# Optimization experiments

Hardware: AMD Instinct MI355X
Metric: run time of the kernel (lower is better)

## Reference

```python
import jax, jax.numpy as jnp
import numpy as np

EPS = 1e-12  # tf.math.l2_normalize epsilon

def _l2_normalize(v, axis):
    sq = jnp.sum(v * v, axis=axis, keepdims=True)
    return v * jax.lax.rsqrt(jnp.maximum(sq, EPS))

def setup_inputs() -> dict:
    key = jax.random.key(0)
    k1, k2, k3 = jax.random.split(key, 3)
    B, H, Wd, Cin, K = 16, 64, 64, 512, 64  # K == dim (required by the source's broadcast)
    x = jax.random.normal(k1, (B, H, Wd, Cin), dtype=jnp.float32)
    W = jax.random.normal(k2, (Cin, K), dtype=jnp.float32) * (1.0 / np.sqrt(Cin))
    b = jnp.zeros((K,), dtype=jnp.float32)
    C = jax.random.uniform(k3, (1, 1, 1, K, K), dtype=jnp.float32)  # [1,1,1,dim,clusters]
    return {"x": x, "W": W, "b": b, "C": C}

def reference(x, W, b, C):
    # 1x1 conv: per-pixel linear projection to cluster logits. NOTE: the
    # original code overwrites x with the conv output, so the VLAD residual
    # is built from these logits, not the input features (faithful to source).
    f = jnp.einsum('bhwc,ck->bhwk', x, W) + b            # [B,H,W,K]
    s = jax.nn.softmax(f, axis=-1)                        # soft assignment over clusters
    # a: [B,H,W,1,K], residual: [B,H,W,dim,K] with dim==K
    v = s[..., None, :] * (f[..., :, None] + C)           # [B,H,W,dim,K]
    v = jnp.sum(v, axis=(1, 2))                           # [B,dim,K]
    v = jnp.transpose(v, (0, 2, 1))                       # [B,K,dim]
    # postnorm=True: intra-normalize per cluster, then global L2 of flattened
    v = _l2_normalize(v, axis=-1)
    flat = v.reshape(v.shape[0], -1)                      # [B, K*dim]
    return _l2_normalize(flat, axis=-1)
```

## Files before the change

kernel.cpp:

```cpp
#include <hip/hip_runtime.h>

#define NB 16
#define HW 4096
#define CIN 512
#define KCL 64
#define BP 128
#define NCHUNK (HW / BP)
#define WT_STRIDE 520
#define FS_STRIDE 68

#define SMEM_FLOATS 17664

typedef short s16x8 __attribute__((ext_vector_type(8)));
typedef float f32x4 __attribute__((ext_vector_type(4)));

__device__ __forceinline__ unsigned short f2bf(float f) {
    unsigned u = __builtin_bit_cast(unsigned, f);
    u += 0x7fffu + ((u >> 16) & 1u);
    return (unsigned short)(u >> 16);
}

__global__ void vlad_prep(const float* __restrict__ Wm, float* __restrict__ A_g,
                          unsigned short* __restrict__ Wt_g)
{
    const int i = blockIdx.x * 256 + threadIdx.x;
    if (i < NB * KCL * KCL + NB * KCL) A_g[i] = 0.f;
    if (i < CIN * KCL) {
        const int k = i >> 6;
        const int n = i & 63;
        Wt_g[n * 512 + k] = f2bf(Wm[i]);
    }
}

__global__ __launch_bounds__(256, 2) void vlad_main(
    const float* __restrict__ x, const unsigned short* __restrict__ Wt_g,
    const float* __restrict__ bv, float* __restrict__ A_g,
    float* __restrict__ sumS_g)
{
    __shared__ float smem_f[SMEM_FLOATS];
    unsigned short* wt = (unsigned short*)smem_f;
    float* fs = smem_f;
    float* ss = smem_f + BP * FS_STRIDE;
    float* sums4 = smem_f + 2 * BP * FS_STRIDE;

    const int t = threadIdx.x;
    const int b = blockIdx.x >> 5;
    const int chunk = blockIdx.x & 31;
    const int pb = b * HW + chunk * BP;

    {
        const int n = t >> 2;
        const int kc = (t & 3) * 128;
        const unsigned short* src = Wt_g + n * 512 + kc;
        unsigned short* dst = wt + n * WT_STRIDE + kc;
#pragma unroll
        for (int i = 0; i < 16; ++i)
            *(float4*)(dst + i * 8) = *(const float4*)(src + i * 8);
    }
    __syncthreads();

    const int wid = t >> 6;
    const int lane = t & 63;
    const int col = lane & 15;
    const int g = lane >> 4;
    const int wpix = pb + wid * 32;

    f32x4 acc[2][4];
#pragma unroll
    for (int mt = 0; mt < 2; ++mt)
#pragma unroll
        for (int nt = 0; nt < 4; ++nt) acc[mt][nt] = (f32x4){0.f, 0.f, 0.f, 0.f};

    const float* xr = x + (size_t)(wpix + col) * CIN + g * 8;
    const unsigned short* wb = wt + col * WT_STRIDE + g * 8;

#pragma unroll
    for (int kk = 0; kk < 16; ++kk) {
        const int k0 = kk * 32;
        s16x8 a[2];
#pragma unroll
        for (int mt = 0; mt < 2; ++mt) {
            const float4 u0 = *(const float4*)(xr + mt * (16 * CIN) + k0);
            const float4 u1 = *(const float4*)(xr + mt * (16 * CIN) + k0 + 4);
            a[mt][0] = (short)f2bf(u0.x); a[mt][1] = (short)f2bf(u0.y);
            a[mt][2] = (short)f2bf(u0.z); a[mt][3] = (short)f2bf(u0.w);
            a[mt][4] = (short)f2bf(u1.x); a[mt][5] = (short)f2bf(u1.y);
            a[mt][6] = (short)f2bf(u1.z); a[mt][7] = (short)f2bf(u1.w);
        }
#pragma unroll
        for (int nt = 0; nt < 4; ++nt) {
            const s16x8 bfr = *(const s16x8*)(wb + nt * (16 * WT_STRIDE) + k0);
            acc[0][nt] = __builtin_amdgcn_mfma_f32_16x16x32_bf16(a[0], bfr, acc[0][nt], 0, 0, 0);
            acc[1][nt] = __builtin_amdgcn_mfma_f32_16x16x32_bf16(a[1], bfr, acc[1][nt], 0, 0, 0);
        }
    }
    __syncthreads();

    float bj[4];
#pragma unroll
    for (int nt = 0; nt < 4; ++nt) bj[nt] = bv[nt * 16 + col];

#pragma unroll
    for (int mt = 0; mt < 2; ++mt)
#pragma unroll
        for (int r = 0; r < 4; ++r) {
            float v0 = acc[mt][0][r] + bj[0];
            float v1 = acc[mt][1][r] + bj[1];
            float v2 = acc[mt][2][r] + bj[2];
            float v3 = acc[mt][3][r] + bj[3];
            float m = fmaxf(fmaxf(v0, v1), fmaxf(v2, v3));
            m = fmaxf(m, __shfl_xor(m, 1));
            m = fmaxf(m, __shfl_xor(m, 2));
            m = fmaxf(m, __shfl_xor(m, 4));
            m = fmaxf(m, __shfl_xor(m, 8));
            const float e0 = __expf(v0 - m);
            const float e1 = __expf(v1 - m);
            const float e2 = __expf(v2 - m);
            const float e3 = __expf(v3 - m);
            float lsum = e0 + e1 + e2 + e3;
            lsum += __shfl_xor(lsum, 1);
            lsum += __shfl_xor(lsum, 2);
            lsum += __shfl_xor(lsum, 4);
            lsum += __shfl_xor(lsum, 8);
            const float rl = 1.0f / lsum;
            const int p = wid * 32 + mt * 16 + g * 4 + r;
            float* fr = fs + p * FS_STRIDE + col;
            fr[0] = v0; fr[16] = v1; fr[32] = v2; fr[48] = v3;
            float* sr = ss + p * FS_STRIDE + col;
            sr[0] = e0 * rl; sr[16] = e1 * rl; sr[32] = e2 * rl; sr[48] = e3 * rl;
        }
    __syncthreads();

    {
        const int c64 = t & 63;
        const int pr = (t >> 6) * 32;
        float sp = 0.f;
#pragma unroll 8
        for (int p = 0; p < 32; ++p) sp += ss[(pr + p) * FS_STRIDE + c64];
        sums4[(t >> 6) * 64 + c64] = sp;
    }

    const int td = t & 15;
    const int tk = t >> 4;
    float Aacc[4][4];
#pragma unroll
    for (int di = 0; di < 4; ++di)
#pragma unroll
        for (int kj = 0; kj < 4; ++kj) Aacc[di][kj] = 0.f;

#pragma unroll 4
    for (int p = 0; p < BP; ++p) {
        const float4 fd = *(const float4*)(fs + p * FS_STRIDE + td * 4);
        const float4 sk = *(const float4*)(ss + p * FS_STRIDE + tk * 4);
        const float fdv[4] = {fd.x, fd.y, fd.z, fd.w};
        const float skv[4] = {sk.x, sk.y, sk.z, sk.w};
#pragma unroll
        for (int di = 0; di < 4; ++di)
#pragma unroll
            for (int kj = 0; kj < 4; ++kj)
                Aacc[di][kj] = fmaf(fdv[di], skv[kj], Aacc[di][kj]);
    }
    __syncthreads();

    float* Ab = A_g + b * (KCL * KCL);
#pragma unroll
    for (int di = 0; di < 4; ++di)
#pragma unroll
        for (int kj = 0; kj < 4; ++kj)
            atomicAdd(Ab + (td * 4 + di) * KCL + tk * 4 + kj, Aacc[di][kj]);

    if (t < 64) {
        const float s4 = sums4[t] + sums4[64 + t] + sums4[128 + t] + sums4[192 + t];
        atomicAdd(sumS_g + b * KCL + t, s4);
    }
}

__global__ __launch_bounds__(256) void vlad_finalize(
    const float* __restrict__ A_g, const float* __restrict__ sumS_g,
    const float* __restrict__ Cm, float* __restrict__ out)
{
    __shared__ float red[4];
    const int b = blockIdx.x;
    const int t = threadIdx.x;
    const int k = t >> 2;
    const int dg = t & 3;
    const float sS = sumS_g[b * 64 + k];
    float v[16];
    float ssq = 0.f;
#pragma unroll
    for (int i = 0; i < 16; ++i) {
        const int d = dg * 16 + i;
        const float val = A_g[((size_t)b * 64 + d) * 64 + k] + Cm[d * 64 + k] * sS;
        v[i] = val;
        ssq += val * val;
    }
    ssq += __shfl_xor(ssq, 1);
    ssq += __shfl_xor(ssq, 2);
    const float rn = rsqrtf(fmaxf(ssq, 1e-12f));
    float gpart = 0.f;
#pragma unroll
    for (int i = 0; i < 16; ++i) {
        v[i] *= rn;
        gpart += v[i] * v[i];
    }
#pragma unroll
    for (int m = 1; m < 64; m <<= 1) gpart += __shfl_xor(gpart, m);
    if ((t & 63) == 0) red[t >> 6] = gpart;
    __syncthreads();
    const float gsq = red[0] + red[1] + red[2] + red[3];
    const float gr = rsqrtf(fmaxf(gsq, 1e-12f));
    float* o = out + (size_t)b * 4096 + k * 64 + dg * 16;
#pragma unroll
    for (int i = 0; i < 16; ++i) o[i] = v[i] * gr;
}

extern "C" void kernel_launch(void* const* d_in, const int* in_sizes, int n_in,
                              void* d_out, int out_size, void* d_ws, size_t ws_size,
                              hipStream_t stream)
{
    const float* x  = (const float*)d_in[0];
    const float* Wm = (const float*)d_in[1];
    const float* bv = (const float*)d_in[2];
    const float* Cm = (const float*)d_in[3];

    float* A_g = (float*)d_ws;
    float* sumS_g = A_g + NB * KCL * KCL;
    unsigned short* Wt_g = (unsigned short*)(sumS_g + NB * KCL);

    const int nz = NB * KCL * KCL + NB * KCL;
    vlad_prep<<<(nz + 255) / 256, 256, 0, stream>>>(Wm, A_g, Wt_g);
    vlad_main<<<NB * NCHUNK, 256, 0, stream>>>(x, Wt_g, bv, A_g, sumS_g);
    vlad_finalize<<<NB, 256, 0, stream>>>(A_g, sumS_g, Cm, (float*)d_out);
}
```

Measured before the change: 228.3 us.

## Use MFMA for per-chunk VLAD aggregation with bf16 transposed LDS tiles

```diff
diff --git a/kernel.cpp b/kernel.cpp
--- a/kernel.cpp
+++ b/kernel.cpp
@@ -1,17 +1,16 @@
 #include <hip/hip_runtime.h>
+#include <hip/hip_bf16.h>
 
 #define NB 16
 #define HW 4096
 #define CIN 512
 #define KCL 64
 #define BP 128
-#define NCHUNK (HW / BP)
-#define WT_STRIDE 520
-#define FS_STRIDE 68
-
-#define SMEM_FLOATS 17664
+#define NCHUNK 32
+#define PSTRIDE 136
 
 typedef short s16x8 __attribute__((ext_vector_type(8)));
+typedef int   i32x4 __attribute__((ext_vector_type(4)));
 typedef float f32x4 __attribute__((ext_vector_type(4)));
 
 __device__ __forceinline__ unsigned short f2bf(float f) {
@@ -20,44 +19,37 @@
     return (unsigned short)(u >> 16);
 }
 
+__device__ __forceinline__ unsigned pk2(float lo, float hi) {
+    __hip_bfloat162 h = __float22bfloat162_rn(make_float2(lo, hi));
+    unsigned r;
+    __builtin_memcpy(&r, &h, 4);
+    return r;
+}
+
 __global__ void vlad_prep(const float* __restrict__ Wm, float* __restrict__ A_g,
                           unsigned short* __restrict__ Wt_g)
 {
     const int i = blockIdx.x * 256 + threadIdx.x;
     if (i < NB * KCL * KCL + NB * KCL) A_g[i] = 0.f;
     if (i < CIN * KCL) {
-        const int k = i >> 6;
+        const int c = i >> 6;
         const int n = i & 63;
-        Wt_g[n * 512 + k] = f2bf(Wm[i]);
-    }
-}
-
-__global__ __launch_bounds__(256, 2) void vlad_main(
+        Wt_g[n * 512 + c] = f2bf(Wm[i]);
+    }
+}
+
+__global__ __launch_bounds__(256, 4) void vlad_main(
     const float* __restrict__ x, const unsigned short* __restrict__ Wt_g,
     const float* __restrict__ bv, float* __restrict__ A_g,
     float* __restrict__ sumS_g)
 {
-    __shared__ float smem_f[SMEM_FLOATS];
-    unsigned short* wt = (unsigned short*)smem_f;
-    float* fs = smem_f;
-    float* ss = smem_f + BP * FS_STRIDE;
-    float* sums4 = smem_f + 2 * BP * FS_STRIDE;
+    __shared__ unsigned short ft[KCL * PSTRIDE];
+    __shared__ unsigned short st[KCL * PSTRIDE];
 
     const int t = threadIdx.x;
     const int b = blockIdx.x >> 5;
     const int chunk = blockIdx.x & 31;
     const int pb = b * HW + chunk * BP;
-
-    {
-        const int n = t >> 2;
-        const int kc = (t & 3) * 128;
-        const unsigned short* src = Wt_g + n * 512 + kc;
-        unsigned short* dst = wt + n * WT_STRIDE + kc;
-#pragma unroll
-        for (int i = 0; i < 16; ++i)
-            *(float4*)(dst + i * 8) = *(const float4*)(src + i * 8);
-    }
-    __syncthreads();
 
     const int wid = t >> 6;
     const int lane = t & 63;
@@ -71,34 +63,38 @@
 #pragma unroll
         for (int nt = 0; nt < 4; ++nt) acc[mt][nt] = (f32x4){0.f, 0.f, 0.f, 0.f};
 
-    const float* xr = x + (size_t)(wpix + col) * CIN + g * 8;
-    const unsigned short* wb = wt + col * WT_STRIDE + g * 8;
+    const float* xr0 = x + (size_t)(wpix + col) * CIN + g * 8;
+    const float* xr1 = xr0 + 16 * CIN;
+    const unsigned short* wbase = Wt_g + col * 512 + g * 8;
 
 #pragma unroll
     for (int kk = 0; kk < 16; ++kk) {
         const int k0 = kk * 32;
-        s16x8 a[2];
-#pragma unroll
-        for (int mt = 0; mt < 2; ++mt) {
-            const float4 u0 = *(const float4*)(xr + mt * (16 * CIN) + k0);
-            const float4 u1 = *(const float4*)(xr + mt * (16 * CIN) + k0 + 4);
-            a[mt][0] = (short)f2bf(u0.x); a[mt][1] = (short)f2bf(u0.y);
-            a[mt][2] = (short)f2bf(u0.z); a[mt][3] = (short)f2bf(u0.w);
-            a[mt][4] = (short)f2bf(u1.x); a[mt][5] = (short)f2bf(u1.y);
-            a[mt][6] = (short)f2bf(u1.z); a[mt][7] = (short)f2bf(u1.w);
+        const float4 u00 = *(const float4*)(xr0 + k0);
+        const float4 u01 = *(const float4*)(xr0 + k0 + 4);
+        const float4 u10 = *(const float4*)(xr1 + k0);
+        const float4 u11 = *(const float4*)(xr1 + k0 + 4);
+        s16x8 wf[4];
+#pragma unroll
+        for (int nt = 0; nt < 4; ++nt)
+            wf[nt] = *(const s16x8*)(wbase + nt * (16 * 512) + k0);
+        const i32x4 a0i = {(int)pk2(u00.x, u00.y), (int)pk2(u00.z, u00.w),
+                           (int)pk2(u01.x, u01.y), (int)pk2(u01.z, u01.w)};
+        const i32x4 a1i = {(int)pk2(u10.x, u10.y), (int)pk2(u10.z, u10.w),
+                           (int)pk2(u11.x, u11.y), (int)pk2(u11.z, u11.w)};
+        const s16x8 a0 = __builtin_bit_cast(s16x8, a0i);
+        const s16x8 a1 = __builtin_bit_cast(s16x8, a1i);
+#pragma unroll
+        for (int nt = 0; nt < 4; ++nt) {
+            acc[0][nt] = __builtin_amdgcn_mfma_f32_16x16x32_bf16(a0, wf[nt], acc[0][nt], 0, 0, 0);
+            acc[1][nt] = __builtin_amdgcn_mfma_f32_16x16x32_bf16(a1, wf[nt], acc[1][nt], 0, 0, 0);
         }
-#pragma unroll
-        for (int nt = 0; nt < 4; ++nt) {
-            const s16x8 bfr = *(const s16x8*)(wb + nt * (16 * WT_STRIDE) + k0);
-            acc[0][nt] = __builtin_amdgcn_mfma_f32_16x16x32_bf16(a[0], bfr, acc[0][nt], 0, 0, 0);
-            acc[1][nt] = __builtin_amdgcn_mfma_f32_16x16x32_bf16(a[1], bfr, acc[1][nt], 0, 0, 0);
-        }
-    }
-    __syncthreads();
+    }
 
     float bj[4];
 #pragma unroll
     for (int nt = 0; nt < 4; ++nt) bj[nt] = bv[nt * 16 + col];
+    float ssum[4] = {0.f, 0.f, 0.f, 0.f};
 
 #pragma unroll
     for (int mt = 0; mt < 2; ++mt)
@@ -123,56 +119,52 @@
             lsum += __shfl_xor(lsum, 4);
             lsum += __shfl_xor(lsum, 8);
             const float rl = 1.0f / lsum;
+            const float s0 = e0 * rl, s1 = e1 * rl, s2 = e2 * rl, s3 = e3 * rl;
+            ssum[0] += s0; ssum[1] += s1; ssum[2] += s2; ssum[3] += s3;
             const int p = wid * 32 + mt * 16 + g * 4 + r;
-            float* fr = fs + p * FS_STRIDE + col;
-            fr[0] = v0; fr[16] = v1; fr[32] = v2; fr[48] = v3;
-            float* sr = ss + p * FS_STRIDE + col;
-            sr[0] = e0 * rl; sr[16] = e1 * rl; sr[32] = e2 * rl; sr[48] = e3 * rl;
+            ft[(col)      * PSTRIDE + p] = f2bf(v0);
+            ft[(col + 16) * PSTRIDE + p] = f2bf(v1);
+            ft[(col + 32) * PSTRIDE + p] = f2bf(v2);
+            ft[(col + 48) * PSTRIDE + p] = f2bf(v3);
+            st[(col)      * PSTRIDE + p] = f2bf(s0);
+            st[(col + 16) * PSTRIDE + p] = f2bf(s1);
+            st[(col + 32) * PSTRIDE + p] = f2bf(s2);
+            st[(col + 48) * PSTRIDE + p] = f2bf(s3);
         }
+
+#pragma unroll
+    for (int nt = 0; nt < 4; ++nt) {
+        ssum[nt] += __shfl_xor(ssum[nt], 16);
+        ssum[nt] += __shfl_xor(ssum[nt], 32);
+    }
+    if (g == 0) {
+#pragma unroll
+        for (int nt = 0; nt < 4; ++nt)
+            atomicAdd(sumS_g + b * KCL + nt * 16 + col, ssum[nt]);
+    }
     __syncthreads();
 
-    {
-        const int c64 = t & 63;
-        const int pr = (t >> 6) * 32;
-        float sp = 0.f;
-#pragma unroll 8
-        for (int p = 0; p < 32; ++p) sp += ss[(pr + p) * FS_STRIDE + c64];
-        sums4[(t >> 6) * 64 + c64] = sp;
-    }
-
-    const int td = t & 15;
-    const int tk = t >> 4;
-    float Aacc[4][4];
-#pragma unroll
-    for (int di = 0; di < 4; ++di)
-#pragma unroll
-        for (int kj = 0; kj < 4; ++kj) Aacc[di][kj] = 0.f;
-
-#pragma unroll 4
-    for (int p = 0; p < BP; ++p) {
-        const float4 fd = *(const float4*)(fs + p * FS_STRIDE + td * 4);
-        const float4 sk = *(const float4*)(ss + p * FS_STRIDE + tk * 4);
-        const float fdv[4] = {fd.x, fd.y, fd.z, fd.w};
-        const float skv[4] = {sk.x, sk.y, sk.z, sk.w};
-#pragma unroll
-        for (int di = 0; di < 4; ++di)
-#pragma unroll
-            for (int kj = 0; kj < 4; ++kj)
-                Aacc[di][kj] = fmaf(fdv[di], skv[kj], Aacc[di][kj]);
-    }
-    __syncthreads();
+    f32x4 acc2[4];
+#pragma unroll
+    for (int nt = 0; nt < 4; ++nt) acc2[nt] = (f32x4){0.f, 0.f, 0.f, 0.f};
+
+    const unsigned short* fta = ft + (wid * 16 + col) * PSTRIDE + g * 8;
+#pragma unroll
+    for (int kk = 0; kk < 4; ++kk) {
+        const s16x8 af = *(const s16x8*)(fta + kk * 32);
+#pragma unroll
+        for (int nt = 0; nt < 4; ++nt) {
+            const s16x8 bf = *(const s16x8*)(st + (nt * 16 + col) * PSTRIDE + kk * 32 + g * 8);
+            acc2[nt] = __builtin_amdgcn_mfma_f32_16x16x32_bf16(af, bf, acc2[nt], 0, 0, 0);
+        }
+    }
 
     float* Ab = A_g + b * (KCL * KCL);
 #pragma unroll
-    for (int di = 0; di < 4; ++di)
-#pragma unroll
-        for (int kj = 0; kj < 4; ++kj)
-            atomicAdd(Ab + (td * 4 + di) * KCL + tk * 4 + kj, Aacc[di][kj]);
-
-    if (t < 64) {
-        const float s4 = sums4[t] + sums4[64 + t] + sums4[128 + t] + sums4[192 + t];
-        atomicAdd(sumS_g + b * KCL + t, s4);
-    }
+    for (int nt = 0; nt < 4; ++nt)
+#pragma unroll
+        for (int r = 0; r < 4; ++r)
+            atomicAdd(Ab + (wid * 16 + g * 4 + r) * KCL + nt * 16 + col, acc2[nt][r]);
 }
 
 __global__ __launch_bounds__(256) void vlad_finalize(
```

Result: faster. 208.7 us (-8.6%).
